# Optimization experiments

Hardware: AMD Instinct MI355X
Metric: run time of the kernel (lower is better)

## Reference

```python
import jax, jax.numpy as jnp
import numpy as np

HIDDEN = 128
INPUT_DIM = 50000


def setup_inputs() -> dict:
    key = jax.random.key(0)
    ks = jax.random.split(key, 9)
    h = HIDDEN
    d = INPUT_DIM

    def lin_init(k, shape, fan_in):
        # equinox Linear/GRUCell default: U(-1/sqrt(fan_in), 1/sqrt(fan_in))
        lim = 1.0 / np.sqrt(fan_in)
        return jax.random.uniform(k, shape, minval=-lim, maxval=lim, dtype=jnp.float32)

    return {
        "x0": jax.random.normal(ks[0], (d,), dtype=jnp.float32),
        "W_enc": lin_init(ks[1], (h, d), d),
        "b_enc": lin_init(ks[2], (h,), d),
        "W_ih": lin_init(ks[3], (3 * h, h), h),
        "W_hh": lin_init(ks[4], (3 * h, h), h),
        "b_ih": lin_init(ks[5], (3 * h,), h),
        "b_n": lin_init(ks[6], (h,), h),
        "W_dec": lin_init(ks[7], (d, h), h),
        "b_dec": lin_init(ks[8], (d,), h),
        "steps": 100,
    }


def _gru_cell(x, h_prev, W_ih, W_hh, b_ih, b_n):
    # equinox eqx.nn.GRUCell math
    ig = jnp.split(W_ih @ x + b_ih, 3)
    hg = jnp.split(W_hh @ h_prev, 3)
    reset = jax.nn.sigmoid(ig[0] + hg[0])
    inp = jax.nn.sigmoid(ig[1] + hg[1])
    new = jnp.tanh(ig[2] + reset * (hg[2] + b_n))
    return new + inp * (h_prev - new)


def reference(x0, W_enc, b_enc, W_ih, W_hh, b_ih, b_n, W_dec, b_dec, steps):
    h0 = jnp.zeros((HIDDEN,), dtype=x0.dtype)

    def scan_step(carry, _):
        h, x_prev = carry
        embedded = W_enc @ x_prev + b_enc            # [hidden]
        h_new = _gru_cell(embedded, h, W_ih, W_hh, b_ih, b_n)
        x_next = W_dec @ h_new + b_dec               # [input_dim]
        return (h_new, x_next), (x_next, x_next, jnp.zeros_like(x_next))

    _, (samples, means, sigmas) = jax.lax.scan(scan_step, (h0, x0), None, length=steps)
    return samples, means, sigmas
```

## Files before the change

kernel.cpp:

```cpp
#include <hip/hip_runtime.h>
#include <math.h>

#define HIDDEN 128
#define IDIM   50000
#define STEPS  100

typedef _Float16 half_t;
typedef _Float16 h2_t __attribute__((ext_vector_type(2)));

#define WS_E1H  0
#define WS_CH   256
#define WS_M    512
#define WS_P    16896
#define WS_Q    66048
#define WS_IG1  66432
#define WS_HT   66816

#define SC_PART 0
#define SC_MP   9000000

__global__ __launch_bounds__(256, 2) void k_encgemm(const float* __restrict__ W_enc,
    const float* __restrict__ W_dec, const float* __restrict__ x0,
    const float* __restrict__ b_dec, float* __restrict__ ws,
    float* __restrict__ scratch)
{
  __shared__ __align__(16) float smem[1024];
  const int t = threadIdx.x;

  if (blockIdx.x < 500){
    float (*As)[128] = (float(*)[128])smem;
    float (*Bs)[128] = (float(*)[128])(smem + 512);
    const int tx = t & 15, ty = t >> 4;
    const int d0 = blockIdx.x * 100;
    const int u  = t - 128, ukk = u >> 5, ug = u & 31;
    float acc[8][8];
    #pragma unroll
    for (int p = 0; p < 8; p++)
      #pragma unroll
      for (int q = 0; q < 8; q++) acc[p][q] = 0.f;

    float4 stage;
    if (t < 128) stage = *(const float4*)(W_enc + (size_t)t*IDIM + d0);
    else         stage = *(const float4*)(W_dec + (size_t)(d0+ukk)*HIDDEN + ug*4);

    for (int k0 = 0; k0 < 100; k0 += 4){
      if (t < 128){
        As[0][t] = stage.x; As[1][t] = stage.y; As[2][t] = stage.z; As[3][t] = stage.w;
      } else {
        *(float4*)&Bs[ukk][ug*4] = stage;
      }
      __syncthreads();
      if (k0 + 4 < 100){
        if (t < 128) stage = *(const float4*)(W_enc + (size_t)t*IDIM + d0 + k0 + 4);
        else         stage = *(const float4*)(W_dec + (size_t)(d0+k0+4+ukk)*HIDDEN + ug*4);
      }
      #pragma unroll
      for (int kk = 0; kk < 4; kk++){
        float4 alo = *(const float4*)&As[kk][ty*8];
        float4 ahi = *(const float4*)&As[kk][ty*8+4];
        float4 blo = *(const float4*)&Bs[kk][tx*8];
        float4 bhi = *(const float4*)&Bs[kk][tx*8+4];
        float a[8] = {alo.x,alo.y,alo.z,alo.w,ahi.x,ahi.y,ahi.z,ahi.w};
        float b[8] = {blo.x,blo.y,blo.z,blo.w,bhi.x,bhi.y,bhi.z,bhi.w};
        #pragma unroll
        for (int p = 0; p < 8; p++)
          #pragma unroll
          for (int q = 0; q < 8; q++) acc[p][q] += a[p]*b[q];
      }
      __syncthreads();
    }
    float* outp = scratch + (size_t)blockIdx.x * 16384;
    #pragma unroll
    for (int p = 0; p < 8; p++){
      #pragma unroll
      for (int q = 0; q < 8; q += 4){
        *(float4*)&outp[(ty*8+p)*128 + tx*8 + q] =
          make_float4(acc[p][q], acc[p][q+1], acc[p][q+2], acc[p][q+3]);
      }
    }
  } else {
    const int bid  = blockIdx.x - 500;
    const int r    = bid >> 1;
    const int half = bid & 1;
    float* r0 = smem;
    float* r1 = smem + 256;
    const float4* wr = (const float4*)(W_enc + (size_t)r*IDIM + half*25000);
    const float4* xv = (const float4*)(x0   + half*25000);
    const float4* bv = (const float4*)(b_dec + half*25000);
    float s0 = 0.f, s1 = 0.f;
    for (int i = t; i < 6250; i += 256){
      float4 w = wr[i]; float4 a = xv[i]; float4 b = bv[i];
      s0 += w.x*a.x + w.y*a.y + w.z*a.z + w.w*a.w;
      s1 += w.x*b.x + w.y*b.y + w.z*b.z + w.w*b.w;
    }
    r0[t] = s0; r1[t] = s1;
    __syncthreads();
    for (int off = 128; off > 0; off >>= 1){
      if (t < off){ r0[t] += r0[t+off]; r1[t] += r1[t+off]; }
      __syncthreads();
    }
    if (t == 0){
      ws[WS_E1H + half*128 + r] = r0[0];
      ws[WS_CH  + half*128 + r] = r1[0];
    }
  }
}

__global__ __launch_bounds__(256) void k_reduce1(const float* __restrict__ scratch,
    float* __restrict__ Mp)
{
  const int g     = blockIdx.x % 10;
  const int chunk = blockIdx.x / 10;
  const int idx   = chunk * 256 + threadIdx.x;
  const float* base = scratch + (size_t)(g*50) * 16384 + idx;
  float s[10];
  #pragma unroll
  for (int uu = 0; uu < 10; uu++) s[uu] = 0.f;
  for (int p = 0; p < 50; p += 10){
    #pragma unroll
    for (int uu = 0; uu < 10; uu++)
      s[uu] += base[(size_t)(p+uu)*16384];
  }
  float t0 = (s[0]+s[1]) + (s[2]+s[3]);
  float t1 = (s[4]+s[5]) + (s[6]+s[7]);
  Mp[(size_t)g*16384 + idx] = t0 + t1 + (s[8]+s[9]);
}

__global__ __launch_bounds__(256) void k_reduce2(const float* __restrict__ Mp,
    float* __restrict__ Mout)
{
  const int idx = blockIdx.x * 256 + threadIdx.x;
  float s = 0.f;
  #pragma unroll
  for (int g = 0; g < 10; g++) s += Mp[(size_t)g*16384 + idx];
  Mout[idx] = s;
}

__global__ __launch_bounds__(128) void k_smallP(const float* __restrict__ W_ih,
    const float* __restrict__ b_ih, const float* __restrict__ b_enc,
    const float* __restrict__ ws, const float* __restrict__ M,
    float* __restrict__ P, float* __restrict__ q, float* __restrict__ ig1)
{
  const int r = blockIdx.x, j = threadIdx.x;
  const float* wr = W_ih + (size_t)r * HIDDEN;
  float acc = 0.f;
  #pragma unroll 8
  for (int k = 0; k < HIDDEN; k++) acc += wr[k] * M[k*HIDDEN + j];
  P[(size_t)r*HIDDEN + j] = acc;
  const float wj = wr[j];
  float cj  = ws[WS_CH  + j] + ws[WS_CH  + 128 + j];
  float e1j = ws[WS_E1H + j] + ws[WS_E1H + 128 + j];
  float t0 = wj * (cj  + b_enc[j]);
  float t1 = wj * (e1j + b_enc[j]);
  __shared__ float r0[128], r1[128];
  r0[j] = t0; r1[j] = t1;
  __syncthreads();
  for (int off = 64; off > 0; off >>= 1){
    if (j < off){ r0[j] += r0[j+off]; r1[j] += r1[j+off]; }
    __syncthreads();
  }
  if (j == 0){
    q[r]   = r0[0] + b_ih[r];
    ig1[r] = r1[0] + b_ih[r];
  }
}

__device__ __forceinline__ float fexp2_(float x){ return __builtin_amdgcn_exp2f(x); }
__device__ __forceinline__ float frcp_(float x){ return __builtin_amdgcn_rcpf(x); }
__device__ __forceinline__ float fsig_(float x){
  return frcp_(1.f + fexp2_(x * -1.44269504f));
}
__device__ __forceinline__ float ftanh_(float x){
  return 1.f - 2.f * frcp_(fexp2_(x * 2.88539008f) + 1.f);
}
__device__ __forceinline__ float dppx1_(float x){
  return __builtin_bit_cast(float,
      __builtin_amdgcn_mov_dpp(__builtin_bit_cast(int, x), 0xB1, 0xF, 0xF, true));
}

__global__
__attribute__((amdgpu_flat_work_group_size(256, 256), amdgpu_waves_per_eu(1, 1)))
void k_recur(const float* __restrict__ P,
    const float* __restrict__ W_hh, const float* __restrict__ q,
    const float* __restrict__ b_n, const float* __restrict__ ig1,
    float* __restrict__ H_T)
{
  const int t = threadIdx.x;
  const int e = t >> 1;
  const int p = t & 1;

  const float* rP0 = P    + (size_t)e         * HIDDEN + p*64;
  const float* rP1 = P    + (size_t)(128 + e) * HIDDEN + p*64;
  const float* rP2 = P    + (size_t)(256 + e) * HIDDEN + p*64;
  const float* rH0 = W_hh + (size_t)e         * HIDDEN + p*64;
  const float* rH1 = W_hh + (size_t)(128 + e) * HIDDEN + p*64;
  const float* rH2 = W_hh + (size_t)(256 + e) * HIDDEN + p*64;

  const float qa = p ? 0.f : q[e];
  const float qb = p ? 0.f : q[128 + e];
  const float qc = p ? 0.f : q[256 + e];

  h2_t wP0[32], wP1[32], wP2[32], wH0[32], wH1[32], wH2[32];
#define LOADROW(DST, SRC)                                                     \
  { const float4* f = (const float4*)(SRC);                                   \
    _Pragma("unroll")                                                         \
    for (int j = 0; j < 16; j++){                                             \
      float4 v = f[j];                                                        \
      h2_t w;                                                                 \
      w.x=(half_t)v.x; w.y=(half_t)v.y; DST[2*j]   = w;                       \
      w.x=(half_t)v.z; w.y=(half_t)v.w; DST[2*j+1] = w;                       \
    } }
  LOADROW(wP0, rP0); LOADROW(wP1, rP1); LOADROW(wP2, rP2);
  LOADROW(wH0, rH0); LOADROW(wH1, rH1); LOADROW(wH2, rH2);
#undef LOADROW

  __shared__ __align__(16) half_t h16[2][HIDDEN];
  __shared__ float Hs[128 * 101];

  const float bn = b_n[e];
  float h;
  {
    float reset = fsig_(ig1[e]);
    float inp   = fsig_(ig1[128 + e]);
    float nw    = ftanh_(ig1[256 + e] + reset * bn);
    h = nw - inp * nw;
  }
  if (!p) h16[0][e] = (half_t)h;
  else    Hs[e * 101] = h;
  __syncthreads();

#define RSTEP(KK, RD, WR)                                                     \
  {                                                                           \
    const uint4* hq = ((const uint4*)(h16[RD])) + p*8;                        \
    float a0 = qa,  a1 = 0.f;               \
    float b0 = qb,  b1 = 0.f;               \
    float c0 = qc,  c1 = 0.f;               \
    float d0 = 0.f, d1 = 0.f;               \
    float g0 = 0.f, g1 = 0.f;               \
    float f0 = 0.f, f1 = 0.f;               \
    _Pragma("unroll")                                                         \
    for (int jj = 0; jj < 8; jj++){                                           \
      uint4 hb = hq[jj];                                                      \
      h2_t hx = __builtin_bit_cast(h2_t, hb.x);                               \
      h2_t hy = __builtin_bit_cast(h2_t, hb.y);                               \
      h2_t hz = __builtin_bit_cast(h2_t, hb.z);                               \
      h2_t hw = __builtin_bit_cast(h2_t, hb.w);                               \
      a0 = __builtin_amdgcn_fdot2(wP0[4*jj+0], hx, a0, false);                \
      a1 = __builtin_amdgcn_fdot2(wP0[4*jj+1], hy, a1, false);                \
      a0 = __builtin_amdgcn_fdot2(wP0[4*jj+2], hz, a0, false);                \
      a1 = __builtin_amdgcn_fdot2(wP0[4*jj+3], hw, a1, false);                \
      b0 = __builtin_amdgcn_fdot2(wP1[4*jj+0], hx, b0, false);                \
      b1 = __builtin_amdgcn_fdot2(wP1[4*jj+1], hy, b1, false);                \
      b0 = __builtin_amdgcn_fdot2(wP1[4*jj+2], hz, b0, false);                \
      b1 = __builtin_amdgcn_fdot2(wP1[4*jj+3], hw, b1, false);                \
      c0 = __builtin_amdgcn_fdot2(wP2[4*jj+0], hx, c0, false);                \
      c1 = __builtin_amdgcn_fdot2(wP2[4*jj+1], hy, c1, false);                \
      c0 = __builtin_amdgcn_fdot2(wP2[4*jj+2], hz, c0, false);                \
      c1 = __builtin_amdgcn_fdot2(wP2[4*jj+3], hw, c1, false);                \
      d0 = __builtin_amdgcn_fdot2(wH0[4*jj+0], hx, d0, false);                \
      d1 = __builtin_amdgcn_fdot2(wH0[4*jj+1], hy, d1, false);                \
      d0 = __builtin_amdgcn_fdot2(wH0[4*jj+2], hz, d0, false);                \
      d1 = __builtin_amdgcn_fdot2(wH0[4*jj+3], hw, d1, false);                \
      g0 = __builtin_amdgcn_fdot2(wH1[4*jj+0], hx, g0, false);                \
      g1 = __builtin_amdgcn_fdot2(wH1[4*jj+1], hy, g1, false);                \
      g0 = __builtin_amdgcn_fdot2(wH1[4*jj+2], hz, g0, false);                \
      g1 = __builtin_amdgcn_fdot2(wH1[4*jj+3], hw, g1, false);                \
      f0 = __builtin_amdgcn_fdot2(wH2[4*jj+0], hx, f0, false);                \
      f1 = __builtin_amdgcn_fdot2(wH2[4*jj+1], hy, f1, false);                \
      f0 = __builtin_amdgcn_fdot2(wH2[4*jj+2], hz, f0, false);                \
      f1 = __builtin_amdgcn_fdot2(wH2[4*jj+3], hw, f1, false);                \
    }                                                                         \
    float A = a0 + a1, B = b0 + b1, C = c0 + c1;                              \
    float D = d0 + d1, G = g0 + g1, F = f0 + f1;                              \
    A += dppx1_(A); B += dppx1_(B); C += dppx1_(C);                           \
    D += dppx1_(D); G += dppx1_(G); F += dppx1_(F);                           \
    float rs = fsig_(A + D);                                                  \
    float ip = fsig_(B + G);                                                  \
    float nw = ftanh_(C + rs * (F + bn));                                     \
    h = nw + ip * (h - nw);                                                   \
    if (!p) h16[WR][e] = (half_t)h;                                           \
    else    Hs[e * 101 + (KK)] = h;                                           \
    __syncthreads();                                                          \
  }

  for (int k = 1; k < STEPS - 1; k += 2){
    RSTEP(k,     0, 1);
    RSTEP(k + 1, 1, 0);
  }
  RSTEP(STEPS - 1, 0, 1);
#undef RSTEP

  for (int i = 0; i < 64; i++){
    int f = i * 256 + t;
    int ee = f >> 7, kk = f & 127;
    H_T[f] = (kk < STEPS) ? Hs[ee * 101 + kk] : 0.f;
  }
}

__global__ __launch_bounds__(256, 4) void k_decode(const float* __restrict__ W_dec,
    const float* __restrict__ b_dec, const float* __restrict__ H_T,
    float* __restrict__ out)
{
  __shared__ __align__(16) float Ws[64][132];
  const int t  = threadIdx.x;
  const int tx = t & 15, ty = t >> 4;
  const int d0 = blockIdx.x * 64;

  #pragma unroll
  for (int i = 0; i < 8; i++){
    int f4 = i * 256 + t;
    int rl = f4 >> 5;
    int cl = (f4 & 31) * 4;
    int rg = d0 + rl;
    float4 v = *(const float4*)&W_dec[(size_t)((rg < IDIM) ? rg : 0)*HIDDEN + cl];
    *(float4*)&Ws[rl][cl] = v;
  }
  __syncthreads();

  float acc[4][8];
  #pragma unroll
  for (int p = 0; p < 4; p++)
    #pragma unroll
    for (int q = 0; q < 8; q++) acc[p][q] = 0.f;

  for (int j0 = 0; j0 < HIDDEN; j0 += 4){
    float4 a0 = *(const float4*)&Ws[tx     ][j0];
    float4 a1 = *(const float4*)&Ws[tx + 16][j0];
    float4 a2 = *(const float4*)&Ws[tx + 32][j0];
    float4 a3 = *(const float4*)&Ws[tx + 48][j0];
    #pragma unroll
    for (int jj = 0; jj < 4; jj++){
      const float* hrow = H_T + (size_t)(j0 + jj) * HIDDEN + ty * 8;
      float4 b0 = *(const float4*)hrow;
      float4 b1 = *(const float4*)(hrow + 4);
      float e0 = (jj==0)?a0.x:(jj==1)?a0.y:(jj==2)?a0.z:a0.w;
      float e1 = (jj==0)?a1.x:(jj==1)?a1.y:(jj==2)?a1.z:a1.w;
      float e2 = (jj==0)?a2.x:(jj==1)?a2.y:(jj==2)?a2.z:a2.w;
      float e3 = (jj==0)?a3.x:(jj==1)?a3.y:(jj==2)?a3.z:a3.w;
      acc[0][0]+=e0*b0.x; acc[0][1]+=e0*b0.y; acc[0][2]+=e0*b0.z; acc[0][3]+=e0*b0.w;
      acc[0][4]+=e0*b1.x; acc[0][5]+=e0*b1.y; acc[0][6]+=e0*b1.z; acc[0][7]+=e0*b1.w;
      acc[1][0]+=e1*b0.x; acc[1][1]+=e1*b0.y; acc[1][2]+=e1*b0.z; acc[1][3]+=e1*b0.w;
      acc[1][4]+=e1*b1.x; acc[1][5]+=e1*b1.y; acc[1][6]+=e1*b1.z; acc[1][7]+=e1*b1.w;
      acc[2][0]+=e2*b0.x; acc[2][1]+=e2*b0.y; acc[2][2]+=e2*b0.z; acc[2][3]+=e2*b0.w;
      acc[2][4]+=e2*b1.x; acc[2][5]+=e2*b1.y; acc[2][6]+=e2*b1.z; acc[2][7]+=e2*b1.w;
      acc[3][0]+=e3*b0.x; acc[3][1]+=e3*b0.y; acc[3][2]+=e3*b0.z; acc[3][3]+=e3*b0.w;
      acc[3][4]+=e3*b1.x; acc[3][5]+=e3*b1.y; acc[3][6]+=e3*b1.z; acc[3][7]+=e3*b1.w;
    }
  }

  bool dv[4]; float bd[4];
  #pragma unroll
  for (int p = 0; p < 4; p++){
    int d = d0 + tx + 16*p;
    dv[p] = (d < IDIM);
    bd[p] = dv[p] ? b_dec[d] : 0.f;
  }
  const size_t SO = (size_t)STEPS * IDIM;
  #pragma unroll
  for (int qq = 0; qq < 8; qq++){
    int k = ty*8 + qq;
    if (k < STEPS){
      size_t o = (size_t)k * IDIM + d0 + tx;
      #pragma unroll
      for (int p = 0; p < 4; p++){
        if (dv[p]){
          float v = acc[p][qq] + bd[p];
          out[o + 16*p]          = v;
          out[o + 16*p + SO]     = v;
          out[o + 16*p + 2*SO]   = 0.f;
        }
      }
    }
  }
}

extern "C" void kernel_launch(void* const* d_in, const int* in_sizes, int n_in,
                              void* d_out, int out_size, void* d_ws, size_t ws_size,
                              hipStream_t stream) {
  const float* x0    = (const float*)d_in[0];
  const float* W_enc = (const float*)d_in[1];
  const float* b_enc = (const float*)d_in[2];
  const float* W_ih  = (const float*)d_in[3];
  const float* W_hh  = (const float*)d_in[4];
  const float* b_ih  = (const float*)d_in[5];
  const float* b_n   = (const float*)d_in[6];
  const float* W_dec = (const float*)d_in[7];
  const float* b_dec = (const float*)d_in[8];
  (void)in_sizes; (void)n_in; (void)out_size; (void)ws_size;

  float* out = (float*)d_out;
  float* ws  = (float*)d_ws;
  float* M   = ws + WS_M;
  float* P   = ws + WS_P;
  float* q   = ws + WS_Q;
  float* ig1 = ws + WS_IG1;
  float* H_T = ws + WS_HT;
  float* scratch = out + SC_PART;
  float* Mp      = out + SC_MP;

  hipLaunchKernelGGL(k_encgemm, dim3(756), dim3(256), 0, stream, W_enc, W_dec, x0, b_dec, ws, scratch);
  hipLaunchKernelGGL(k_reduce1, dim3(640), dim3(256), 0, stream, scratch, Mp);
  hipLaunchKernelGGL(k_reduce2, dim3(64),  dim3(256), 0, stream, Mp, M);
  hipLaunchKernelGGL(k_smallP,  dim3(384), dim3(128), 0, stream, W_ih, b_ih, b_enc, ws, M, P, q, ig1);
  hipLaunchKernelGGL(k_recur,   dim3(1),   dim3(256), 0, stream, P, W_hh, q, b_n, ig1, H_T);
  hipLaunchKernelGGL(k_decode,  dim3(782), dim3(256), 0, stream, W_dec, b_dec, H_T, out);
}
```

Baseline: 267.4 us.

## Remap decode GEMM so each lane owns one output row for coalesced stores

The decode kernel's thread mapping changes. Each lane now owns one input-dim row and each of the four waves covers 25 timesteps, replacing the 4x8 register tile over 16x16 threads. Output stores become fully coalesced 64-wide rows per timestep, and the zero-padded steps 100-127 are no longer computed. The shared-memory row pad is now 129 to avoid bank conflicts on scalar row reads. H_T values are wave-uniform scalar loads, but each W element is now reused across only 25 accumulators, and the loads use strided scalar addressing.

Measured after the change: 251.7 us. 1.06x faster.

```diff
diff --git a/kernel.cpp b/kernel.cpp
--- a/kernel.cpp
+++ b/kernel.cpp
@@ -301,10 +301,12 @@
     const float* __restrict__ b_dec, const float* __restrict__ H_T,
     float* __restrict__ out)
 {
-  __shared__ __align__(16) float Ws[64][132];
-  const int t  = threadIdx.x;
-  const int tx = t & 15, ty = t >> 4;
-  const int d0 = blockIdx.x * 64;
+  __shared__ float Ws[64 * 129];
+  const int t    = threadIdx.x;
+  const int lane = t & 63;
+  const int wv   = __builtin_amdgcn_readfirstlane(t >> 6);
+  const int d0   = blockIdx.x * 64;
+  const int d    = d0 + lane;
 
   #pragma unroll
   for (int i = 0; i < 8; i++){
@@ -312,64 +314,39 @@
     int rl = f4 >> 5;
     int cl = (f4 & 31) * 4;
     int rg = d0 + rl;
-    float4 v = *(const float4*)&W_dec[(size_t)((rg < IDIM) ? rg : 0)*HIDDEN + cl];
-    *(float4*)&Ws[rl][cl] = v;
+    float4 v = *(const float4*)&W_dec[(size_t)((rg < IDIM) ? rg : (IDIM-1))*HIDDEN + cl];
+    Ws[rl*129 + cl + 0] = v.x;
+    Ws[rl*129 + cl + 1] = v.y;
+    Ws[rl*129 + cl + 2] = v.z;
+    Ws[rl*129 + cl + 3] = v.w;
   }
   __syncthreads();
 
-  float acc[4][8];
+  const int k0 = wv * 25;
+  float acc[25];
   #pragma unroll
-  for (int p = 0; p < 4; p++)
-    #pragma unroll
-    for (int q = 0; q < 8; q++) acc[p][q] = 0.f;
-
-  for (int j0 = 0; j0 < HIDDEN; j0 += 4){
-    float4 a0 = *(const float4*)&Ws[tx     ][j0];
-    float4 a1 = *(const float4*)&Ws[tx + 16][j0];
-    float4 a2 = *(const float4*)&Ws[tx + 32][j0];
-    float4 a3 = *(const float4*)&Ws[tx + 48][j0];
-    #pragma unroll
-    for (int jj = 0; jj < 4; jj++){
-      const float* hrow = H_T + (size_t)(j0 + jj) * HIDDEN + ty * 8;
-      float4 b0 = *(const float4*)hrow;
-      float4 b1 = *(const float4*)(hrow + 4);
-      float e0 = (jj==0)?a0.x:(jj==1)?a0.y:(jj==2)?a0.z:a0.w;
-      float e1 = (jj==0)?a1.x:(jj==1)?a1.y:(jj==2)?a1.z:a1.w;
-      float e2 = (jj==0)?a2.x:(jj==1)?a2.y:(jj==2)?a2.z:a2.w;
-      float e3 = (jj==0)?a3.x:(jj==1)?a3.y:(jj==2)?a3.z:a3.w;
-      acc[0][0]+=e0*b0.x; acc[0][1]+=e0*b0.y; acc[0][2]+=e0*b0.z; acc[0][3]+=e0*b0.w;
-      acc[0][4]+=e0*b1.x; acc[0][5]+=e0*b1.y; acc[0][6]+=e0*b1.z; acc[0][7]+=e0*b1.w;
-      acc[1][0]+=e1*b0.x; acc[1][1]+=e1*b0.y; acc[1][2]+=e1*b0.z; acc[1][3]+=e1*b0.w;
-      acc[1][4]+=e1*b1.x; acc[1][5]+=e1*b1.y; acc[1][6]+=e1*b1.z; acc[1][7]+=e1*b1.w;
-      acc[2][0]+=e2*b0.x; acc[2][1]+=e2*b0.y; acc[2][2]+=e2*b0.z; acc[2][3]+=e2*b0.w;
-      acc[2][4]+=e2*b1.x; acc[2][5]+=e2*b1.y; acc[2][6]+=e2*b1.z; acc[2][7]+=e2*b1.w;
-      acc[3][0]+=e3*b0.x; acc[3][1]+=e3*b0.y; acc[3][2]+=e3*b0.z; acc[3][3]+=e3*b0.w;
-      acc[3][4]+=e3*b1.x; acc[3][5]+=e3*b1.y; acc[3][6]+=e3*b1.z; acc[3][7]+=e3*b1.w;
-    }
-  }
-
-  bool dv[4]; float bd[4];
-  #pragma unroll
-  for (int p = 0; p < 4; p++){
-    int d = d0 + tx + 16*p;
-    dv[p] = (d < IDIM);
-    bd[p] = dv[p] ? b_dec[d] : 0.f;
-  }
-  const size_t SO = (size_t)STEPS * IDIM;
-  #pragma unroll
-  for (int qq = 0; qq < 8; qq++){
-    int k = ty*8 + qq;
-    if (k < STEPS){
-      size_t o = (size_t)k * IDIM + d0 + tx;
-      #pragma unroll
-      for (int p = 0; p < 4; p++){
-        if (dv[p]){
-          float v = acc[p][qq] + bd[p];
-          out[o + 16*p]          = v;
-          out[o + 16*p + SO]     = v;
-          out[o + 16*p + 2*SO]   = 0.f;
-        }
-      }
+  for (int k = 0; k < 25; k++) acc[k] = 0.f;
+
+  const float* wrow = &Ws[lane * 129];
+  #pragma unroll 2
+  for (int j = 0; j < HIDDEN; j++){
+    float w = wrow[j];
+    const float* hp = &H_T[j * HIDDEN + k0];
+    #pragma unroll
+    for (int k = 0; k < 25; k++)
+      acc[k] = fmaf(w, hp[k], acc[k]);
+  }
+
+  if (d < IDIM){
+    const float bd = b_dec[d];
+    const size_t SO = (size_t)STEPS * IDIM;
+    #pragma unroll
+    for (int k = 0; k < 25; k++){
+      float v = acc[k] + bd;
+      size_t o = (size_t)(k0 + k) * IDIM + d;
+      out[o]        = v;
+      out[o + SO]   = v;
+      out[o + 2*SO] = 0.f;
     }
   }
 }
```
